# Kernel tuning notes

Measured on AMD Instinct MI355X. Metric: run time of the kernel, lower is better.

Reference implementation:

```python
import jax, jax.numpy as jnp
import numpy as np

B, N, M, DIM, H, DH = 2, 2048, 2048, 1024, 16, 64
INNER = H * DH


def setup_inputs() -> dict:
    key = jax.random.key(0)
    ks = jax.random.split(key, 6)
    x = jax.random.normal(ks[0], (B, N, DIM), dtype=jnp.float32)
    cond = jax.random.normal(ks[1], (B, M, DIM), dtype=jnp.float32)
    mask = jax.random.randint(ks[2], (B, M), 0, 2) > 0
    s = 0.02
    Wq = jax.random.normal(ks[3], (DIM, INNER), dtype=jnp.float32) * s
    Wkv = jax.random.normal(ks[4], (DIM, 2 * INNER), dtype=jnp.float32) * s
    Wo = jax.random.normal(ks[5], (INNER, DIM), dtype=jnp.float32) * s
    bo = jnp.zeros((DIM,), dtype=jnp.float32)
    return {"x": x, "cond": cond, "mask": mask, "Wq": Wq, "Wkv": Wkv, "Wo": Wo, "bo": bo}


def reference(x, cond, mask, Wq, Wkv, Wo, bo):
    b, n, _ = x.shape
    m = cond.shape[1]
    scale = DH ** -0.5
    # projections
    q = (x @ Wq).reshape(b, n, H, DH).transpose(0, 2, 1, 3)  # b h n d
    kv = cond @ Wkv
    k, v = jnp.split(kv, 2, axis=-1)
    k = k.reshape(b, m, H, DH).transpose(0, 2, 1, 3)
    v = v.reshape(b, m, H, DH).transpose(0, 2, 1, 3)
    q = q * scale
    dots = jnp.einsum('bhid,bhjd->bhij', q, k)  # b h n m
    neg = -jnp.finfo(dots.dtype).max
    # padding mask: [b, j] -> [b, 1, 1, j]
    dots = jnp.where(mask[:, None, None, :], dots, neg)
    # causal mask: triu with offset j - i + 1
    causal = jnp.triu(jnp.ones((n, m), dtype=bool), k=m - n + 1)
    dots = jnp.where(causal[None, None, :, :], neg, dots)
    attn = jax.nn.softmax(dots, axis=-1)
    out = jnp.einsum('bhij,bhjd->bhid', attn, v)  # b h n d
    out = out.transpose(0, 2, 1, 3).reshape(b, n, INNER)
    return out @ Wo + bo
```

## Files before the change

### kernel.cpp

```cpp
#include <hip/hip_runtime.h>
#include <float.h>


typedef __bf16 bf16x8 __attribute__((ext_vector_type(8)));
typedef __bf16 bf16x4 __attribute__((ext_vector_type(4)));
typedef float f32x4 __attribute__((ext_vector_type(4)));
typedef unsigned short u16x4 __attribute__((ext_vector_type(4)));
typedef short s16x4 __attribute__((ext_vector_type(4)));

#define DEV static __device__ __forceinline__

DEV unsigned short f2bf(float f) {
  union { float f; unsigned u; } v; v.f = f;
  unsigned r = v.u + 0x7FFFu + ((v.u >> 16) & 1u);
  return (unsigned short)(r >> 16);
}
DEV float bf2f(unsigned short u) {
  union { unsigned u; float f; } v; v.u = ((unsigned)u) << 16; return v.f;
}
DEV bf16x8 ldb8(const unsigned short* p) { return *reinterpret_cast<const bf16x8*>(p); }
DEV bf16x4 ldb4(const unsigned short* p) { return *reinterpret_cast<const bf16x4*>(p); }
DEV f32x4 zero4() { f32x4 z = {0.f, 0.f, 0.f, 0.f}; return z; }

DEV f32x4 mfma32(bf16x8 a, bf16x8 b, f32x4 c) {
  return __builtin_amdgcn_mfma_f32_16x16x32_bf16(a, b, c, 0, 0, 0);
}
#if __has_builtin(__builtin_amdgcn_mfma_f32_16x16x16_bf16)
DEV f32x4 mfma16(bf16x4 a, bf16x4 b, f32x4 c) {
  return __builtin_amdgcn_mfma_f32_16x16x16_bf16(a, b, c, 0, 0, 0);
}
#else
DEV f32x4 mfma16(bf16x4 a, bf16x4 b, f32x4 c) {
  return __builtin_amdgcn_mfma_f32_16x16x16bf16_1k(
      __builtin_bit_cast(s16x4, a), __builtin_bit_cast(s16x4, b), c, 0, 0, 0);
}
#endif
#if __has_builtin(__builtin_amdgcn_exp2f)
DEV float fexp2(float x) { return __builtin_amdgcn_exp2f(x); }
#else
DEV float fexp2(float x) { return exp2f(x); }
#endif

DEV void gload16(const void* g, void* l) {
  __builtin_amdgcn_global_load_lds(
      (const __attribute__((address_space(1))) unsigned int*)g,
      (__attribute__((address_space(3))) unsigned int*)l, 16, 0, 0);
}

#define QSCALE 0.1803368801111354f

__global__ __launch_bounds__(256) void cast2_kernel(const float* __restrict__ x,
                                                    const float* __restrict__ cond,
                                                    unsigned short* __restrict__ xb,
                                                    unsigned short* __restrict__ condb) {
  const bool second = blockIdx.x >= 4096;
  const float* in = second ? cond : x;
  unsigned short* out = second ? condb : xb;
  int t = (blockIdx.x & 4095) * 256 + threadIdx.x;
  f32x4 v = *reinterpret_cast<const f32x4*>(in + (size_t)t * 4);
  u16x4 o;
  o[0] = f2bf(v[0]); o[1] = f2bf(v[1]); o[2] = f2bf(v[2]); o[3] = f2bf(v[3]);
  *reinterpret_cast<u16x4*>(out + (size_t)t * 4) = o;
}

__global__ __launch_bounds__(256) void transpose3_kernel(
    const float* __restrict__ Wq, const float* __restrict__ Wkv, const float* __restrict__ Wo,
    unsigned short* __restrict__ WqT, unsigned short* __restrict__ WkvT,
    unsigned short* __restrict__ WoT) {
  __shared__ float tile[64][65];
  int bid = blockIdx.x;
  const float* in; unsigned short* out; int N_;
  if (bid < 256)      { in = Wq;  out = WqT;  N_ = 1024; }
  else if (bid < 768) { in = Wkv; out = WkvT; N_ = 2048; bid -= 256; }
  else                { in = Wo;  out = WoT;  N_ = 1024; bid -= 768; }
  const int tx = bid & ((N_ >> 6) - 1);
  const int ty = bid / (N_ >> 6);
  const int n0 = tx << 6, k0 = ty << 6;
  const int c = threadIdx.x & 63, r4 = threadIdx.x >> 6;
#pragma unroll
  for (int i = 0; i < 16; ++i) {
    const int r = r4 + i * 4;
    tile[r][c] = in[(size_t)(k0 + r) * N_ + n0 + c];
  }
  __syncthreads();
#pragma unroll
  for (int i = 0; i < 16; ++i) {
    const int r = r4 * 16 + i;
    out[(size_t)(n0 + r) * 1024 + k0 + c] = f2bf(tile[c][r]);
  }
}

DEV void gemm_core(const unsigned short* __restrict__ Ap, const unsigned short* __restrict__ Bp,
                   unsigned short* As, unsigned short* Bs, f32x4 (&acc)[4][4]) {
  const int tid = threadIdx.x;
  const int lane = tid & 63, w = tid >> 6;
  const int li = lane & 15, hi = lane >> 4;
  const int wr = w >> 1, wc = w & 1;
  const int rA = lane >> 2;
  const int cs = lane & 3;
  const int slot = cs ^ (rA & 3);
  const unsigned short* a0 = Ap + (size_t)(w * 16 + rA) * 1024 + slot * 8;
  const unsigned short* a1 = Ap + (size_t)(w * 16 + 64 + rA) * 1024 + slot * 8;
  const unsigned short* b0 = Bp + (size_t)(w * 16 + rA) * 1024 + slot * 8;
  const unsigned short* b1 = Bp + (size_t)(w * 16 + 64 + rA) * 1024 + slot * 8;
  unsigned short* lA0 = As + (w * 16) * 32;
  unsigned short* lA1 = As + (w * 16 + 64) * 32;
  unsigned short* lB0 = Bs + (w * 16) * 32;
  unsigned short* lB1 = Bs + (w * 16 + 64) * 32;
  const int fsl = (hi ^ (li & 3)) * 8;

  for (int kt = 0; kt < 1024; kt += 32) {
    __syncthreads();
    gload16(a0 + kt, lA0);
    gload16(a1 + kt, lA1);
    gload16(b0 + kt, lB0);
    gload16(b1 + kt, lB1);
    __syncthreads();
    bf16x8 af[4], bfv[4];
#pragma unroll
    for (int i = 0; i < 4; ++i) {
      af[i]  = *reinterpret_cast<const bf16x8*>(As + (wr * 64 + i * 16 + li) * 32 + fsl);
      bfv[i] = *reinterpret_cast<const bf16x8*>(Bs + (wc * 64 + i * 16 + li) * 32 + fsl);
    }
#pragma unroll
    for (int mi = 0; mi < 4; ++mi)
#pragma unroll
      for (int ni = 0; ni < 4; ++ni)
        acc[mi][ni] = mfma32(af[mi], bfv[ni], acc[mi][ni]);
  }
}

__global__ __launch_bounds__(256, 3) void gemm_qkv(const unsigned short* __restrict__ xb,
                                                   const unsigned short* __restrict__ condb,
                                                   const unsigned short* __restrict__ WqT,
                                                   const unsigned short* __restrict__ WkvT,
                                                   unsigned short* __restrict__ Qb,
                                                   unsigned short* __restrict__ Kb,
                                                   unsigned short* __restrict__ Vt) {
  __shared__ unsigned short As[128 * 32], Bs[128 * 32];
  const int bid = blockIdx.x;
  const bool isQ = bid < 256;
  int gm0, gn0;
  const unsigned short *Ap, *Bp;
  if (isQ) {
    gm0 = (bid >> 3) * 128; gn0 = (bid & 7) * 128;
    Ap = xb + (size_t)gm0 * 1024; Bp = WqT + (size_t)gn0 * 1024;
  } else {
    const int id = bid - 256;
    gm0 = (id >> 4) * 128; gn0 = (id & 15) * 128;
    Ap = condb + (size_t)gm0 * 1024; Bp = WkvT + (size_t)gn0 * 1024;
  }
  f32x4 acc[4][4];
#pragma unroll
  for (int i = 0; i < 4; ++i)
#pragma unroll
    for (int j = 0; j < 4; ++j) acc[i][j] = zero4();
  gemm_core(Ap, Bp, As, Bs, acc);

  const int lane = threadIdx.x & 63;
  const int w = threadIdx.x >> 6;
  const int li = lane & 15, hi = lane >> 4;
  const int wm0 = gm0 + (w >> 1) * 64;
  const int wn0 = gn0 + (w & 1) * 64;
#pragma unroll
  for (int mi = 0; mi < 4; ++mi) {
#pragma unroll
    for (int ni = 0; ni < 4; ++ni) {
      const int gc = wn0 + ni * 16 + li;
#pragma unroll
      for (int r = 0; r < 4; ++r) {
        const int gm = wm0 + mi * 16 + 4 * hi + r;
        float v = acc[mi][ni][r];
        const int b = gm >> 11, mr = gm & 2047;
        if (isQ) {
          v *= QSCALE;
          const int hh = gc >> 6, d = gc & 63;
          Qb[((size_t)((b << 4) + hh) * 2048 + mr) * 64 + d] = f2bf(v);
        } else if (gc < 1024) {
          const int hh = gc >> 6, d = gc & 63;
          Kb[((size_t)((b << 4) + hh) * 2048 + mr) * 64 + d] = f2bf(v);
        } else {
          const int c2 = gc - 1024, hh = c2 >> 6, d = c2 & 63;
          Vt[(size_t)((b << 4) + hh) * 131072 + (size_t)d * 2048 + mr] = f2bf(v);
        }
      }
    }
  }
}

__global__ __launch_bounds__(256, 3) void gemm_o(const unsigned short* __restrict__ Ob,
                                                 const unsigned short* __restrict__ WoT,
                                                 float* __restrict__ oF,
                                                 const float* __restrict__ bias) {
  __shared__ unsigned short As[128 * 32], Bs[128 * 32];
  const int gm0 = (blockIdx.x >> 3) * 128, gn0 = (blockIdx.x & 7) * 128;
  f32x4 acc[4][4];
#pragma unroll
  for (int i = 0; i < 4; ++i)
#pragma unroll
    for (int j = 0; j < 4; ++j) acc[i][j] = zero4();
  gemm_core(Ob + (size_t)gm0 * 1024, WoT + (size_t)gn0 * 1024, As, Bs, acc);

  const int lane = threadIdx.x & 63;
  const int w = threadIdx.x >> 6;
  const int li = lane & 15, hi = lane >> 4;
  const int wm0 = gm0 + (w >> 1) * 64;
  const int wn0 = gn0 + (w & 1) * 64;
#pragma unroll
  for (int mi = 0; mi < 4; ++mi) {
#pragma unroll
    for (int ni = 0; ni < 4; ++ni) {
      const int gc = wn0 + ni * 16 + li;
#pragma unroll
      for (int r = 0; r < 4; ++r) {
        const int gm = wm0 + mi * 16 + 4 * hi + r;
        oF[(size_t)gm * 1024 + gc] = acc[mi][ni][r] + bias[gc];
      }
    }
  }
}

__global__ __launch_bounds__(256) void vmean_mask_kernel(const unsigned short* __restrict__ Vt,
                                                         const int* __restrict__ mask,
                                                         float* __restrict__ Vmean,
                                                         float* __restrict__ maskf) {
  if (blockIdx.x < 16) {
    const int idx = blockIdx.x * 256 + threadIdx.x;
    maskf[idx] = mask[idx] ? 1.f : 0.f;
  }
  const int bh = blockIdx.x;
  const int t = threadIdx.x;
  const int d = t >> 2, part = t & 3;
  const unsigned short* p = Vt + (size_t)bh * 131072 + (size_t)d * 2048 + part * 512;
  float s = 0.f;
  for (int i = 0; i < 512; i += 4) {
    u16x4 v = *reinterpret_cast<const u16x4*>(p + i);
    s += bf2f(v[0]) + bf2f(v[1]) + bf2f(v[2]) + bf2f(v[3]);
  }
  __shared__ float red[256];
  red[t] = s;
  __syncthreads();
  if (part == 0)
    Vmean[bh * 64 + d] = (red[t] + red[t + 1] + red[t + 2] + red[t + 3]) * (1.f / 2048.f);
}

__global__ __launch_bounds__(256, 4) void attn_kernel(const unsigned short* __restrict__ Qb,
                                                      const unsigned short* __restrict__ Kb,
                                                      const unsigned short* __restrict__ Vt,
                                                      const float* __restrict__ maskf,
                                                      const float* __restrict__ Vmean,
                                                      unsigned short* __restrict__ O) {
  __shared__ unsigned short lds[16384];
  const int bid = blockIdx.x;
  const int xcd = bid & 7;
  const int s = bid >> 3;
  const int bh = (xcd << 2) + (s >> 4);
  const int t15 = s & 15;
  const int qc = (t15 & 1) ? (t15 >> 1) : (15 - (t15 >> 1));
  const int tid = threadIdx.x;
  const int w = tid >> 6;
  const int lane = tid & 63;
  const int li = lane & 15, hi = lane >> 4;
  const int qw0 = (qc << 7) + (w << 5);
  const int b = bh >> 4;

  const unsigned short* Qp = Qb + (size_t)bh * 131072 + (size_t)qw0 * 64;
  const unsigned short* Kp = Kb + (size_t)bh * 131072;
  const unsigned short* Vp = Vt + (size_t)bh * 131072;
  const float* mp = maskf + b * 2048;

  const int g0 = tid, g1 = tid + 256;
  const int r0 = g0 >> 3, r1 = g1 >> 3;
  const int sc0 = ((g0 & 7) ^ (r0 & 7)) * 8, sc1 = ((g1 & 7) ^ (r1 & 7)) * 8;
  const unsigned short* ks0 = Kp + r0 * 64 + sc0;
  const unsigned short* ks1 = Kp + r1 * 64 + sc1;
  const unsigned short* vs0 = Vp + (size_t)r0 * 2048 + sc0;
  const unsigned short* vs1 = Vp + (size_t)r1 * 2048 + sc1;
  const int wd = w * 512;

  const int kg0 = (hi ^ (li & 7)) << 3;
  int vpre[4];
#pragma unroll
  for (int ks = 0; ks < 4; ++ks)
    vpre[ks] = (((2 * ks + (hi >> 1)) ^ (li & 7)) << 3) + ((hi & 1) << 2);

  bf16x8 qf[2][2];
#pragma unroll
  for (int g = 0; g < 2; ++g) {
    qf[g][0] = ldb8(Qp + (g * 16 + li) * 64 + hi * 8);
    qf[g][1] = ldb8(Qp + (g * 16 + li) * 64 + 32 + hi * 8);
  }

  f32x4 o[2][4];
#pragma unroll
  for (int g = 0; g < 2; ++g)
#pragma unroll
    for (int n = 0; n < 4; ++n) o[g][n] = zero4();
  float lp[2] = {0.f, 0.f};

  const int ntiles = 2 * qc + 2;

  gload16(ks0, lds + wd);
  gload16(ks1, lds + 2048 + wd);
  gload16(vs0, lds + 8192 + wd);
  gload16(vs1, lds + 8192 + 2048 + wd);
  __syncthreads();

  int buf = 0;
  for (int t = 0; t < ntiles; ++t) {
    if (t + 1 < ntiles) {
      const int nb = (buf ^ 1) * 4096;
      const int koff = (t + 1) * 4096;
      const int voff = (t + 1) * 64;
      gload16(ks0 + koff, lds + nb + wd);
      gload16(ks1 + koff, lds + nb + 2048 + wd);
      gload16(vs0 + voff, lds + 8192 + nb + wd);
      gload16(vs1 + voff, lds + 8192 + nb + 2048 + wd);
    }
    const unsigned short* kl = lds + buf * 4096;
    const unsigned short* vl = lds + 8192 + buf * 4096;
#pragma unroll
    for (int s2 = 0; s2 < 2; ++s2) {
      const int kv0s = t * 64 + s2 * 32;
      const int rb = (s2 * 32 + li) * 64;
      const bf16x8 k00 = ldb8(kl + rb + kg0);
      const bf16x8 k01 = ldb8(kl + rb + (kg0 ^ 32));
      const bf16x8 k10 = ldb8(kl + rb + 1024 + kg0);
      const bf16x8 k11 = ldb8(kl + rb + 1024 + (kg0 ^ 32));
      bf16x4 vb[4][2];
#pragma unroll
      for (int d0 = 0; d0 < 4; ++d0) {
        vb[d0][0] = ldb4(vl + (d0 * 16 + li) * 64 + vpre[2 * s2 + 0]);
        vb[d0][1] = ldb4(vl + (d0 * 16 + li) * 64 + vpre[2 * s2 + 1]);
      }
      const f32x4 mf0 = *reinterpret_cast<const f32x4*>(mp + kv0s + 4 * hi);
      const f32x4 mf1 = *reinterpret_cast<const f32x4*>(mp + kv0s + 16 + 4 * hi);
#pragma unroll
      for (int g = 0; g < 2; ++g) {
        f32x4 st0 = zero4(), st1 = zero4();
        st0 = mfma32(k00, qf[g][0], st0);
        st0 = mfma32(k01, qf[g][1], st0);
        st1 = mfma32(k10, qf[g][0], st1);
        st1 = mfma32(k11, qf[g][1], st1);
        const int q = qw0 + g * 16 + li;
        float p0[4], p1[4];
#pragma unroll
        for (int r = 0; r < 4; ++r) {
          const float f = (kv0s + 4 * hi + r <= q) ? mf0[r] : 0.f;
          p0[r] = fexp2(st0[r]) * f;
        }
#pragma unroll
        for (int r = 0; r < 4; ++r) {
          const float f = (kv0s + 16 + 4 * hi + r <= q) ? mf1[r] : 0.f;
          p1[r] = fexp2(st1[r]) * f;
        }
        lp[g] += (p0[0] + p0[1]) + (p0[2] + p0[3]) + (p1[0] + p1[1]) + (p1[2] + p1[3]);
        bf16x4 pa0, pa1;
#pragma unroll
        for (int r = 0; r < 4; ++r) { pa0[r] = (__bf16)p0[r]; pa1[r] = (__bf16)p1[r]; }
#pragma unroll
        for (int d0 = 0; d0 < 4; ++d0) {
          o[g][d0] = mfma16(pa0, vb[d0][0], o[g][d0]);
          o[g][d0] = mfma16(pa1, vb[d0][1], o[g][d0]);
        }
      }
    }
    __syncthreads();
    buf ^= 1;
  }

  float lt[2];
#pragma unroll
  for (int g = 0; g < 2; ++g) {
    float v = lp[g];
    v += __shfl_xor(v, 16, 64);
    v += __shfl_xor(v, 32, 64);
    lt[g] = v;
  }

  const int h = bh & 15;
#pragma unroll
  for (int g = 0; g < 2; ++g) {
    unsigned short* Op = O + ((size_t)(b * 2048 + qw0 + g * 16)) * 1024 + h * 64;
#pragma unroll
    for (int r = 0; r < 4; ++r) {
      const int qrow = 4 * hi + r;
      const float ls = __shfl(lt[g], qrow, 64);
      const bool dead = (ls == 0.f);
      const float inv = dead ? 0.f : (1.f / ls);
      const float v0 = dead ? Vmean[bh * 64 + 0 + li] : o[g][0][r] * inv;
      const float v1 = dead ? Vmean[bh * 64 + 16 + li] : o[g][1][r] * inv;
      const float v2 = dead ? Vmean[bh * 64 + 32 + li] : o[g][2][r] * inv;
      const float v3 = dead ? Vmean[bh * 64 + 48 + li] : o[g][3][r] * inv;
      unsigned short* row = Op + (size_t)qrow * 1024;
      row[0 + li] = f2bf(v0);
      row[16 + li] = f2bf(v1);
      row[32 + li] = f2bf(v2);
      row[48 + li] = f2bf(v3);
    }
  }
}

extern "C" void kernel_launch(void* const* d_in, const int* in_sizes, int n_in,
                              void* d_out, int out_size, void* d_ws, size_t ws_size,
                              hipStream_t stream) {
  const float* x    = (const float*)d_in[0];
  const float* cond = (const float*)d_in[1];
  const int*   mask = (const int*)d_in[2];
  const float* Wq   = (const float*)d_in[3];
  const float* Wkv  = (const float*)d_in[4];
  const float* Wo   = (const float*)d_in[5];
  const float* bo   = (const float*)d_in[6];
  float* out = (float*)d_out;

  char* ws = (char*)d_ws;
  const size_t MB = 1u << 20;
  unsigned short* xb    = (unsigned short*)(ws + 0 * MB);
  unsigned short* condb = (unsigned short*)(ws + 8 * MB);
  unsigned short* WqT   = (unsigned short*)(ws + 16 * MB);
  unsigned short* WkvT  = (unsigned short*)(ws + 18 * MB);
  unsigned short* WoT   = (unsigned short*)(ws + 22 * MB);
  unsigned short* Qb    = (unsigned short*)(ws + 24 * MB);
  unsigned short* Kb    = (unsigned short*)(ws + 32 * MB);
  unsigned short* Vt    = (unsigned short*)(ws + 40 * MB);
  unsigned short* Ob    = (unsigned short*)(ws + 48 * MB);
  float*          Vmean = (float*)(ws + 56 * MB);
  float*          maskf = (float*)(ws + 56 * MB + 8192);
  (void)in_sizes; (void)n_in; (void)out_size; (void)ws_size;

  cast2_kernel<<<8192, 256, 0, stream>>>(x, cond, xb, condb);
  transpose3_kernel<<<1024, 256, 0, stream>>>(Wq, Wkv, Wo, WqT, WkvT, WoT);
  gemm_qkv<<<768, 256, 0, stream>>>(xb, condb, WqT, WkvT, Qb, Kb, Vt);
  vmean_mask_kernel<<<32, 256, 0, stream>>>(Vt, mask, Vmean, maskf);
  attn_kernel<<<512, 256, 0, stream>>>(Qb, Kb, Vt, maskf, Vmean, Ob);
  gemm_o<<<256, 256, 0, stream>>>(Ob, WoT, out, bo);
}
```

Baseline: 274.4 us.

## Split attention into 64-row query blocks with 128 threads and prefetch mask

The attention kernel now launches 1024 blocks of 128 threads, each covering 64 query rows instead of 128, with a new balanced causal scheduling that pairs short and long query chunks per XCD. Each thread now issues four K and four V async loads per tile to fill the same 64-key LDS tile. The mask values for the next tile are prefetched into registers alongside the K/V loads. The goal is better load balance and more blocks in flight for the causal triangle, at the cost of more per-block K/V reloads, since each block reuses K/V across fewer query rows.

```diff
diff --git a/kernel.cpp b/kernel.cpp
--- a/kernel.cpp
+++ b/kernel.cpp
@@ -244,7 +244,7 @@
     Vmean[bh * 64 + d] = (red[t] + red[t + 1] + red[t + 2] + red[t + 3]) * (1.f / 2048.f);
 }
 
-__global__ __launch_bounds__(256, 4) void attn_kernel(const unsigned short* __restrict__ Qb,
+__global__ __launch_bounds__(128, 2) void attn_kernel(const unsigned short* __restrict__ Qb,
                                                       const unsigned short* __restrict__ Kb,
                                                       const unsigned short* __restrict__ Vt,
                                                       const float* __restrict__ maskf,
@@ -254,14 +254,15 @@
   const int bid = blockIdx.x;
   const int xcd = bid & 7;
   const int s = bid >> 3;
-  const int bh = (xcd << 2) + (s >> 4);
-  const int t15 = s & 15;
-  const int qc = (t15 & 1) ? (t15 >> 1) : (15 - (t15 >> 1));
+  const int u = s & 31, v = s >> 5;
+  const int beta = u & 3, base = u >> 2;
+  const int c = (v & 1) ? (31 - base - ((v >> 1) << 3)) : (base + ((v >> 1) << 3));
+  const int bh = (xcd << 2) + beta;
   const int tid = threadIdx.x;
   const int w = tid >> 6;
   const int lane = tid & 63;
   const int li = lane & 15, hi = lane >> 4;
-  const int qw0 = (qc << 7) + (w << 5);
+  const int qw0 = (c << 6) + (w << 5);
   const int b = bh >> 4;
 
   const unsigned short* Qp = Qb + (size_t)bh * 131072 + (size_t)qw0 * 64;
@@ -269,14 +270,16 @@
   const unsigned short* Vp = Vt + (size_t)bh * 131072;
   const float* mp = maskf + b * 2048;
 
-  const int g0 = tid, g1 = tid + 256;
-  const int r0 = g0 >> 3, r1 = g1 >> 3;
-  const int sc0 = ((g0 & 7) ^ (r0 & 7)) * 8, sc1 = ((g1 & 7) ^ (r1 & 7)) * 8;
-  const unsigned short* ks0 = Kp + r0 * 64 + sc0;
-  const unsigned short* ks1 = Kp + r1 * 64 + sc1;
-  const unsigned short* vs0 = Vp + (size_t)r0 * 2048 + sc0;
-  const unsigned short* vs1 = Vp + (size_t)r1 * 2048 + sc1;
-  const int wd = w * 512;
+  const unsigned short* ksrc[4];
+  const unsigned short* vsrc[4];
+#pragma unroll
+  for (int i = 0; i < 4; ++i) {
+    const int g = i * 128 + tid;
+    const int r = g >> 3;
+    const int slot = (g & 7) ^ (r & 7);
+    ksrc[i] = Kp + r * 64 + slot * 8;
+    vsrc[i] = Vp + (size_t)r * 2048 + slot * 8;
+  }
 
   const int kg0 = (hi ^ (li & 7)) << 3;
   int vpre[4];
@@ -298,12 +301,16 @@
     for (int n = 0; n < 4; ++n) o[g][n] = zero4();
   float lp[2] = {0.f, 0.f};
 
-  const int ntiles = 2 * qc + 2;
-
-  gload16(ks0, lds + wd);
-  gload16(ks1, lds + 2048 + wd);
-  gload16(vs0, lds + 8192 + wd);
-  gload16(vs1, lds + 8192 + 2048 + wd);
+  const int ntiles = c + 1;
+
+#pragma unroll
+  for (int i = 0; i < 4; ++i) gload16(ksrc[i], lds + i * 1024 + w * 512);
+#pragma unroll
+  for (int i = 0; i < 4; ++i) gload16(vsrc[i], lds + 8192 + i * 1024 + w * 512);
+  f32x4 mcur[4], mnext[4];
+#pragma unroll
+  for (int j = 0; j < 4; ++j)
+    mcur[j] = *reinterpret_cast<const f32x4*>(mp + j * 16 + 4 * hi);
   __syncthreads();
 
   int buf = 0;
@@ -312,10 +319,13 @@
       const int nb = (buf ^ 1) * 4096;
       const int koff = (t + 1) * 4096;
       const int voff = (t + 1) * 64;
-      gload16(ks0 + koff, lds + nb + wd);
-      gload16(ks1 + koff, lds + nb + 2048 + wd);
-      gload16(vs0 + voff, lds + 8192 + nb + wd);
-      gload16(vs1 + voff, lds + 8192 + nb + 2048 + wd);
+#pragma unroll
+      for (int i = 0; i < 4; ++i) gload16(ksrc[i] + koff, lds + nb + i * 1024 + w * 512);
+#pragma unroll
+      for (int i = 0; i < 4; ++i) gload16(vsrc[i] + voff, lds + 8192 + nb + i * 1024 + w * 512);
+#pragma unroll
+      for (int j = 0; j < 4; ++j)
+        mnext[j] = *reinterpret_cast<const f32x4*>(mp + (t + 1) * 64 + j * 16 + 4 * hi);
     }
     const unsigned short* kl = lds + buf * 4096;
     const unsigned short* vl = lds + 8192 + buf * 4096;
@@ -333,8 +343,8 @@
         vb[d0][0] = ldb4(vl + (d0 * 16 + li) * 64 + vpre[2 * s2 + 0]);
         vb[d0][1] = ldb4(vl + (d0 * 16 + li) * 64 + vpre[2 * s2 + 1]);
       }
-      const f32x4 mf0 = *reinterpret_cast<const f32x4*>(mp + kv0s + 4 * hi);
-      const f32x4 mf1 = *reinterpret_cast<const f32x4*>(mp + kv0s + 16 + 4 * hi);
+      const f32x4 mf0 = mcur[2 * s2 + 0];
+      const f32x4 mf1 = mcur[2 * s2 + 1];
 #pragma unroll
       for (int g = 0; g < 2; ++g) {
         f32x4 st0 = zero4(), st1 = zero4();
@@ -367,15 +377,17 @@
     }
     __syncthreads();
     buf ^= 1;
+#pragma unroll
+    for (int j = 0; j < 4; ++j) mcur[j] = mnext[j];
   }
 
   float lt[2];
 #pragma unroll
   for (int g = 0; g < 2; ++g) {
-    float v = lp[g];
-    v += __shfl_xor(v, 16, 64);
-    v += __shfl_xor(v, 32, 64);
-    lt[g] = v;
+    float vv = lp[g];
+    vv += __shfl_xor(vv, 16, 64);
+    vv += __shfl_xor(vv, 32, 64);
+    lt[g] = vv;
   }
 
   const int h = bh & 15;
@@ -432,6 +444,6 @@
   transpose3_kernel<<<1024, 256, 0, stream>>>(Wq, Wkv, Wo, WqT, WkvT, WoT);
   gemm_qkv<<<768, 256, 0, stream>>>(xb, condb, WqT, WkvT, Qb, Kb, Vt);
   vmean_mask_kernel<<<32, 256, 0, stream>>>(Vt, mask, Vmean, maskf);
-  attn_kernel<<<512, 256, 0, stream>>>(Qb, Kb, Vt, maskf, Vmean, Ob);
+  attn_kernel<<<1024, 128, 0, stream>>>(Qb, Kb, Vt, maskf, Vmean, Ob);
   gemm_o<<<256, 256, 0, stream>>>(Ob, WoT, out, bo);
 }
```

After: 232.5 us. 1.18x faster.
